# Kernel optimization log

Measured on AMD Instinct MI355X. Metric: run time of the kernel, lower is better.

Reference implementation:

```python
import jax, jax.numpy as jnp
import numpy as np

B, L, D, H = 2, 2048, 1024, 16
Dh = D // H

def setup_inputs() -> dict:
    key = jax.random.key(0)
    kx, kq, kk, kv, ko = jax.random.split(key, 5)
    scale = 1.0 / np.sqrt(D)
    return {
        "x": jax.random.normal(kx, (B, L, D), dtype=jnp.float32),
        "Wq": jax.random.normal(kq, (D, H, Dh), dtype=jnp.float32) * scale,
        "Wk": jax.random.normal(kk, (D, H, Dh), dtype=jnp.float32) * scale,
        "Wv": jax.random.normal(kv, (D, H, Dh), dtype=jnp.float32) * scale,
        "Wout": jax.random.normal(ko, (H, Dh, D), dtype=jnp.float32) * (1.0 / np.sqrt(D)),
    }

def reference(x, Wq, Wk, Wv, Wout):
    # QKV projections: [B,L,D] x [D,H,Dh] -> [B,L,H,Dh]
    q = jnp.einsum('bld,dhe->blhe', x, Wq)
    k = jnp.einsum('bld,dhe->blhe', x, Wk)
    v = jnp.einsum('bld,dhe->blhe', x, Wv)
    # scores [B,H,L,L]
    a = jnp.einsum('bqhd,bkhd->bhqk', q, k) / (Dh ** 0.5)
    Lq = x.shape[1]
    mask = jnp.tril(jnp.ones((1, 1, Lq, Lq), dtype=jnp.bool_))
    NEG_INF = jnp.finfo(jnp.float32).min
    a = jnp.where(mask, a, NEG_INF)
    a = jax.nn.softmax(a, axis=-1)
    o = jnp.einsum('bhqk,bkhd->bqhd', a, v)
    # output projection: [B,L,H,Dh] x [H,Dh,D] -> [B,L,D]
    return jnp.einsum('blhe,hed->bld', o, Wout)
```

## Files before the change

kernel.cpp:

```cpp
#include <hip/hip_runtime.h>

typedef __bf16 bf16x8 __attribute__((ext_vector_type(8)));
typedef __bf16 bf16x4 __attribute__((ext_vector_type(4)));
typedef float  floatx4 __attribute__((ext_vector_type(4)));

constexpr int Bc = 2, Lc = 2048, Dc = 1024, Hc = 16, Dhc = 64;
constexpr int Mr = 4096;

__device__ __forceinline__ void gl_lds16(const void* g, void* l) {
  __builtin_amdgcn_global_load_lds(
      (const __attribute__((address_space(1))) void*)g,
      (__attribute__((address_space(3))) void*)l, 16, 0, 0);
}

__global__ __launch_bounds__(256) void k_pack_rows(const float* __restrict__ X,
                                                   __bf16* __restrict__ P) {
  __shared__ __align__(16) __bf16 tile[64][32];
  int t = threadIdx.x;
  int m0 = blockIdx.x * 64, p0 = blockIdx.y * 4;
  int r = t >> 2, cc = t & 3;
  const float4* src = (const float4*)&X[(size_t)(m0 + r) * 1024 + p0 * 8 + cc * 8];
  float4 v0 = src[0], v1 = src[1];
  bf16x8 o;
  o[0] = (__bf16)v0.x; o[1] = (__bf16)v0.y; o[2] = (__bf16)v0.z; o[3] = (__bf16)v0.w;
  o[4] = (__bf16)v1.x; o[5] = (__bf16)v1.y; o[6] = (__bf16)v1.z; o[7] = (__bf16)v1.w;
  *(bf16x8*)&tile[r][cc * 8] = o;
  __syncthreads();
  int pc = t >> 6, ml = t & 63;
  bf16x8 q = *(bf16x8*)&tile[ml][pc * 8];
  *(bf16x8*)&P[((size_t)(p0 + pc) * Mr + m0 + ml) * 8] = q;
}

__global__ __launch_bounds__(256) void k_pack_T4(const float* __restrict__ W0,
                                                 const float* __restrict__ W1,
                                                 const float* __restrict__ W2,
                                                 const float* __restrict__ W3,
                                                 __bf16* __restrict__ Pall) {
  int z = blockIdx.z;
  const float* W = (z == 0) ? W0 : (z == 1) ? W1 : (z == 2) ? W2 : W3;
  __bf16* P = Pall + (size_t)z * 1024 * 1024;
  __shared__ __align__(16) __bf16 tile[64][66];
  int t = threadIdx.x;
  int k0 = blockIdx.x * 64, n0 = blockIdx.y * 64;
  int r = t >> 2, cc = t & 3;
  const float4* src = (const float4*)&W[(size_t)(k0 + r) * 1024 + n0 + cc * 16];
#pragma unroll
  for (int i = 0; i < 4; i++) {
    float4 v = src[i];
    tile[r][cc * 16 + i * 4 + 0] = (__bf16)v.x;
    tile[r][cc * 16 + i * 4 + 1] = (__bf16)v.y;
    tile[r][cc * 16 + i * 4 + 2] = (__bf16)v.z;
    tile[r][cc * 16 + i * 4 + 3] = (__bf16)v.w;
  }
  __syncthreads();
#pragma unroll
  for (int i = 0; i < 2; i++) {
    int c = t + i * 256;
    int pl = c >> 6, nl = c & 63;
    bf16x8 o;
#pragma unroll
    for (int j = 0; j < 8; j++) o[j] = tile[pl * 8 + j][nl];
    *(bf16x8*)&P[((size_t)(k0 / 8 + pl) * 1024 + n0 + nl) * 8] = o;
  }
}

template <int MODE, int AM>
__global__ __launch_bounds__(256) void k_gemm(const __bf16* __restrict__ Ap8,
                                              const __bf16* __restrict__ Bp8,
                                              float* __restrict__ outF,
                                              __bf16* __restrict__ Qb,
                                              __bf16* __restrict__ Kb,
                                              __bf16* __restrict__ Vb) {
  constexpr int K = 1024;
  constexpr int KCB = 2080;
  __shared__ __align__(16) char smem[4 * KCB * 4];
  char* As_raw = smem;
  char* Bs_raw = smem + 4 * KCB;
  int t = threadIdx.x, lane = t & 63, w = t >> 6;
  int quad = lane >> 4, l16 = lane & 15;
  int m0 = blockIdx.x * 128;
  const __bf16* Bbase;
  int n0loc, mat = 0;
  if (MODE == 1) {
    mat = blockIdx.y >> 3;
    Bbase = Bp8 + (size_t)mat * 1024 * 1024;
    n0loc = (blockIdx.y & 7) * 128;
  } else {
    Bbase = Bp8;
    n0loc = blockIdx.y * 128;
  }
  int wm = (w & 1) * 64, wn = (w >> 1) * 64;
  floatx4 acc[4][4] = {};

  for (int k0 = 0; k0 < K; k0 += 32) {
    int kp = k0 >> 3;
    const __bf16* ga = Ap8 + ((size_t)(kp + w) * AM + m0 + lane) * 8;
    const __bf16* gb = Bbase + ((size_t)(kp + w) * 1024 + n0loc + lane) * 8;
    char* la = As_raw + w * KCB;
    char* lb = Bs_raw + w * KCB;
    __syncthreads();
    gl_lds16(ga, la);
    gl_lds16(ga + 512, la + 1024);
    gl_lds16(gb, lb);
    gl_lds16(gb + 512, lb + 1024);
    __syncthreads();
    bf16x8 af[4], bfv[4];
#pragma unroll
    for (int mi = 0; mi < 4; mi++)
      af[mi] = *(const bf16x8*)(As_raw + quad * KCB + (wm + mi * 16 + l16) * 16);
#pragma unroll
    for (int ni = 0; ni < 4; ni++)
      bfv[ni] = *(const bf16x8*)(Bs_raw + quad * KCB + (wn + ni * 16 + l16) * 16);
#pragma unroll
    for (int mi = 0; mi < 4; mi++)
#pragma unroll
      for (int ni = 0; ni < 4; ni++)
        acc[mi][ni] = __builtin_amdgcn_mfma_f32_16x16x32_bf16(af[mi], bfv[ni], acc[mi][ni], 0, 0, 0);
  }

  __syncthreads();

  if (MODE == 0) {
    float* slf = (float*)(smem + w * (4 * KCB));
#pragma unroll
    for (int nh = 0; nh < 2; nh++) {
#pragma unroll
      for (int mi = 0; mi < 4; mi++)
#pragma unroll
        for (int nin = 0; nin < 2; nin++)
#pragma unroll
          for (int r = 0; r < 4; r++) {
            int l_loc = mi * 16 + quad * 4 + r;
            int c_loc = nin * 16 + l16;
            slf[l_loc * 32 + c_loc] = acc[mi][nh * 2 + nin][r];
          }
      __builtin_amdgcn_s_waitcnt(0);
#pragma unroll
      for (int i = 0; i < 8; i++) {
        int c = i * 64 + lane;
        float4 v = *(float4*)((char*)slf + c * 16);
        int row = c >> 3, sub = c & 7;
        *(float4*)&outF[(size_t)(m0 + wm + row) * 1024 + n0loc + wn + nh * 32 + sub * 4] = v;
      }
      if (nh == 0) __builtin_amdgcn_s_waitcnt(0);
    }
  } else {
    __bf16* sl = (__bf16*)(smem + w * (4 * KCB));
    int b = (m0 + wm) >> 11;
    int lbase = (m0 + wm) & 2047;
    int h = (n0loc + wn) >> 6;
    int bh2 = b * 16 + h;
    __bf16* dst;
    float scl = 1.0f;
    if (mat == 0) {
      dst = Qb + (((size_t)(bh2 * 64 + (lbase >> 5)) * 4) << 9);
      scl = 0.18033688011112042f;
    } else if (mat == 1) {
      dst = Kb + (((size_t)(bh2 * 32 + (lbase >> 6)) * 8) << 9);
    } else {
      dst = Vb + (((size_t)(bh2 * 32 + (lbase >> 6)) * 8) << 9);
    }
#pragma unroll
    for (int mi = 0; mi < 4; mi++)
#pragma unroll
      for (int ni = 0; ni < 4; ni++)
#pragma unroll
        for (int r = 0; r < 4; r++) {
          int l_loc = mi * 16 + quad * 4 + r;
          int e = ni * 16 + l16;
          int off;
          if (mat == 0)
            off = ((l_loc >> 5) * 4 + ((l_loc >> 4) & 1) * 2 + (e >> 5)) * 512 +
                  (((e >> 3) & 3) * 16 + (l_loc & 15)) * 8 + (e & 7);
          else if (mat == 1)
            off = ((l_loc >> 4) * 2 + (e >> 5)) * 512 +
                  (((e >> 3) & 3) * 16 + (l_loc & 15)) * 8 + (e & 7);
          else
            off = ((e >> 4) * 2 + (l_loc >> 5)) * 512 +
                  (((l_loc >> 2) & 3) * 16 + (e & 15)) * 8 + ((l_loc >> 4) & 1) * 4 + (l_loc & 3);
          sl[off] = (__bf16)(acc[mi][ni][r] * scl);
        }
    __builtin_amdgcn_s_waitcnt(0);
#pragma unroll
    for (int i = 0; i < 8; i++) {
      int c = i * 64 + lane;
      bf16x8 v = *(bf16x8*)(sl + c * 8);
      *(bf16x8*)(dst + c * 8) = v;
    }
  }
}

__global__ __launch_bounds__(256) void k_attn(const __bf16* __restrict__ Qf,
                                              const __bf16* __restrict__ Kf,
                                              const __bf16* __restrict__ Vf,
                                              __bf16* __restrict__ Op8) {
  __shared__ float PO[4][64][33];
  __shared__ float Pl[4][2][16];
  int t = threadIdx.x;
  int lane = t & 63, w = t >> 6;
  int quad = lane >> 4, l16 = lane & 15;
  int bid = blockIdx.x;
  int xcd = bid & 7, g = bid >> 3;
  int bh = xcd * 4 + (g & 3);
  int qt = 63 - (g >> 2);
  int qbase = qt * 32;

  const __bf16* Qp = Qf + (((size_t)(bh * 64 + qt) * 4) << 9) + lane * 8;
  bf16x8 qf[2][2];
#pragma unroll
  for (int mi = 0; mi < 2; mi++)
#pragma unroll
    for (int kk = 0; kk < 2; kk++)
      qf[mi][kk] = *(const bf16x8*)(Qp + ((mi * 2 + kk) << 9));

  floatx4 ot[4][2] = {};
  float l_s[2] = {0.f, 0.f};

  auto do_tile = [&](int kt, bool domask) {
    int kbase = kt * 64;
    const __bf16* Kp = Kf + (((size_t)(bh * 32 + kt) * 8) << 9) + lane * 8;
    const __bf16* Vp = Vf + (((size_t)(bh * 32 + kt) * 8) << 9) + lane * 8;
    bf16x8 ka[4][2], va[4][2];
#pragma unroll
    for (int kb = 0; kb < 4; kb++)
#pragma unroll
      for (int kk = 0; kk < 2; kk++) {
        ka[kb][kk] = *(const bf16x8*)(Kp + ((kb * 2 + kk) << 9));
        va[kb][kk] = *(const bf16x8*)(Vp + ((kb * 2 + kk) << 9));
      }

    floatx4 st[4][2] = {};
#pragma unroll
    for (int kb = 0; kb < 4; kb++)
#pragma unroll
      for (int mi = 0; mi < 2; mi++) {
        st[kb][mi] = __builtin_amdgcn_mfma_f32_16x16x32_bf16(ka[kb][0], qf[mi][0], st[kb][mi], 0, 0, 0);
        st[kb][mi] = __builtin_amdgcn_mfma_f32_16x16x32_bf16(ka[kb][1], qf[mi][1], st[kb][mi], 0, 0, 0);
      }

    bf16x8 pb[2][2];
#pragma unroll
    for (int mi = 0; mi < 2; mi++) {
      int q_g = qbase + mi * 16 + l16;
      float pv[4][4];
      float psum = 0.f;
#pragma unroll
      for (int kb = 0; kb < 4; kb++)
#pragma unroll
        for (int r = 0; r < 4; r++) {
          float v = st[kb][mi][r];
          if (domask) {
            int key = kbase + kb * 16 + quad * 4 + r;
            if (key > q_g) v = -__builtin_inff();
          }
          float p = __builtin_amdgcn_exp2f(v);
          pv[kb][r] = p;
          psum += p;
        }
      l_s[mi] += psum;
#pragma unroll
      for (int kp = 0; kp < 2; kp++) {
        bf16x8 p8;
#pragma unroll
        for (int j = 0; j < 4; j++) {
          p8[j] = (__bf16)pv[kp * 2][j];
          p8[j + 4] = (__bf16)pv[kp * 2 + 1][j];
        }
        pb[mi][kp] = p8;
      }
    }

#pragma unroll
    for (int kbd = 0; kbd < 4; kbd++)
#pragma unroll
      for (int mi = 0; mi < 2; mi++) {
        ot[kbd][mi] = __builtin_amdgcn_mfma_f32_16x16x32_bf16(va[kbd][0], pb[mi][0], ot[kbd][mi], 0, 0, 0);
        ot[kbd][mi] = __builtin_amdgcn_mfma_f32_16x16x32_bf16(va[kbd][1], pb[mi][1], ot[kbd][mi], 0, 0, 0);
      }
  };

  int nkt = ((qt * 32 + 31) >> 6) + 1;
  for (int kt = w; kt < nkt - 1; kt += 4) do_tile(kt, false);
  if (((nkt - 1) & 3) == w) do_tile(nkt - 1, true);

#pragma unroll
  for (int mi = 0; mi < 2; mi++) {
    l_s[mi] += __shfl_xor(l_s[mi], 16);
    l_s[mi] += __shfl_xor(l_s[mi], 32);
  }

#pragma unroll
  for (int mi = 0; mi < 2; mi++) {
    if (quad == 0) Pl[w][mi][l16] = l_s[mi];
#pragma unroll
    for (int kbd = 0; kbd < 4; kbd++)
#pragma unroll
      for (int r = 0; r < 4; r++)
        PO[w][kbd * 16 + quad * 4 + r][mi * 16 + l16] = ot[kbd][mi][r];
  }
  __syncthreads();

  int oct = lane >> 3, rl = lane & 7;
  int ql = w * 8 + rl;
  float lstar = 0.f;
#pragma unroll
  for (int ww = 0; ww < 4; ww++) lstar += Pl[ww][ql >> 4][ql & 15];
  float inv = 1.f / lstar;
  bf16x8 ov;
#pragma unroll
  for (int j = 0; j < 8; j++) {
    float accv = 0.f;
#pragma unroll
    for (int ww = 0; ww < 4; ww++) accv += PO[ww][oct * 8 + j][ql];
    ov[j] = (__bf16)(accv * inv);
  }
  int b = bh >> 4, h = bh & 15;
  size_t row = (size_t)b * Lc + qbase + ql;
  *(bf16x8*)&Op8[((size_t)(h * 8 + oct) * Mr + row) * 8] = ov;
}

extern "C" void kernel_launch(void* const* d_in, const int* in_sizes, int n_in,
                              void* d_out, int out_size, void* d_ws, size_t ws_size,
                              hipStream_t stream) {
  const float* x  = (const float*)d_in[0];
  const float* Wq = (const float*)d_in[1];
  const float* Wk = (const float*)d_in[2];
  const float* Wv = (const float*)d_in[3];
  const float* Wo = (const float*)d_in[4];
  float* out = (float*)d_out;

  if (ws_size < (size_t)50331648) return;
  __bf16* xb   = (__bf16*)d_ws;
  __bf16* wqkv = xb + (size_t)Mr * Dc;
  __bf16* wot  = wqkv + (size_t)3 * Dc * Dc;
  __bf16* Qfr  = wot + (size_t)Dc * Dc;
  __bf16* Kfr  = Qfr + (size_t)Mr * Dc;
  __bf16* Vfr  = Kfr + (size_t)Mr * Dc;
  __bf16* Op8  = Vfr + (size_t)Mr * Dc;

  k_pack_rows<<<dim3(64, 32), 256, 0, stream>>>(x, xb);
  k_pack_T4<<<dim3(16, 16, 4), 256, 0, stream>>>(Wq, Wk, Wv, Wo, wqkv);

  k_gemm<1, Mr><<<dim3(32, 24), 256, 0, stream>>>(xb, wqkv, nullptr, Qfr, Kfr, Vfr);

  k_attn<<<dim3(2048), 256, 0, stream>>>(Qfr, Kfr, Vfr, Op8);

  k_gemm<0, Mr><<<dim3(32, 8), 256, 0, stream>>>(Op8, wot, out, nullptr, nullptr, nullptr);
}
```

Measured before the change: 168.1 us.

## Merge pack kernels, retile output GEMM, shrink attention reduction LDS

The two packing kernels become one launch indexed by a flat block id, which removes a launch. The output-projection GEMM is split into its own kernel with 128x64 tiles, doubling the grid from 256 to 512 blocks to fill more CUs. The attention kernel's cross-wave partial-output reduction moves from a padded fp32 LDS buffer to a bf16 transposed buffer read as 8-wide vectors, and gets a launch_bounds occupancy hint of 5. The bf16 partials add rounding error before the final sum.

```diff
diff --git a/kernel.cpp b/kernel.cpp
--- a/kernel.cpp
+++ b/kernel.cpp
@@ -13,64 +13,63 @@
       (__attribute__((address_space(3))) void*)l, 16, 0, 0);
 }
 
-__global__ __launch_bounds__(256) void k_pack_rows(const float* __restrict__ X,
-                                                   __bf16* __restrict__ P) {
-  __shared__ __align__(16) __bf16 tile[64][32];
+__global__ __launch_bounds__(256) void k_pack(const float* __restrict__ X,
+                                              const float* __restrict__ W0,
+                                              const float* __restrict__ W1,
+                                              const float* __restrict__ W2,
+                                              const float* __restrict__ W3,
+                                              __bf16* __restrict__ Pw,
+                                              __bf16* __restrict__ Px) {
+  __shared__ __align__(16) __bf16 tile[64][66];
+  int bid = blockIdx.x;
   int t = threadIdx.x;
-  int m0 = blockIdx.x * 64, p0 = blockIdx.y * 4;
-  int r = t >> 2, cc = t & 3;
-  const float4* src = (const float4*)&X[(size_t)(m0 + r) * 1024 + p0 * 8 + cc * 8];
-  float4 v0 = src[0], v1 = src[1];
-  bf16x8 o;
-  o[0] = (__bf16)v0.x; o[1] = (__bf16)v0.y; o[2] = (__bf16)v0.z; o[3] = (__bf16)v0.w;
-  o[4] = (__bf16)v1.x; o[5] = (__bf16)v1.y; o[6] = (__bf16)v1.z; o[7] = (__bf16)v1.w;
-  *(bf16x8*)&tile[r][cc * 8] = o;
-  __syncthreads();
-  int pc = t >> 6, ml = t & 63;
-  bf16x8 q = *(bf16x8*)&tile[ml][pc * 8];
-  *(bf16x8*)&P[((size_t)(p0 + pc) * Mr + m0 + ml) * 8] = q;
-}
-
-__global__ __launch_bounds__(256) void k_pack_T4(const float* __restrict__ W0,
-                                                 const float* __restrict__ W1,
-                                                 const float* __restrict__ W2,
-                                                 const float* __restrict__ W3,
-                                                 __bf16* __restrict__ Pall) {
-  int z = blockIdx.z;
-  const float* W = (z == 0) ? W0 : (z == 1) ? W1 : (z == 2) ? W2 : W3;
-  __bf16* P = Pall + (size_t)z * 1024 * 1024;
-  __shared__ __align__(16) __bf16 tile[64][66];
-  int t = threadIdx.x;
-  int k0 = blockIdx.x * 64, n0 = blockIdx.y * 64;
-  int r = t >> 2, cc = t & 3;
-  const float4* src = (const float4*)&W[(size_t)(k0 + r) * 1024 + n0 + cc * 16];
-#pragma unroll
-  for (int i = 0; i < 4; i++) {
-    float4 v = src[i];
-    tile[r][cc * 16 + i * 4 + 0] = (__bf16)v.x;
-    tile[r][cc * 16 + i * 4 + 1] = (__bf16)v.y;
-    tile[r][cc * 16 + i * 4 + 2] = (__bf16)v.z;
-    tile[r][cc * 16 + i * 4 + 3] = (__bf16)v.w;
-  }
-  __syncthreads();
-#pragma unroll
-  for (int i = 0; i < 2; i++) {
-    int c = t + i * 256;
-    int pl = c >> 6, nl = c & 63;
+  if (bid < 1024) {
+    int z = bid >> 8, rem = bid & 255;
+    int k0 = (rem & 15) << 6, n0 = (rem >> 4) << 6;
+    const float* W = (z == 0) ? W0 : (z == 1) ? W1 : (z == 2) ? W2 : W3;
+    __bf16* P = Pw + (size_t)z * 1024 * 1024;
+    int r = t >> 2, cc = t & 3;
+    const float4* src = (const float4*)&W[(size_t)(k0 + r) * 1024 + n0 + cc * 16];
+#pragma unroll
+    for (int i = 0; i < 4; i++) {
+      float4 v = src[i];
+      tile[r][cc * 16 + i * 4 + 0] = (__bf16)v.x;
+      tile[r][cc * 16 + i * 4 + 1] = (__bf16)v.y;
+      tile[r][cc * 16 + i * 4 + 2] = (__bf16)v.z;
+      tile[r][cc * 16 + i * 4 + 3] = (__bf16)v.w;
+    }
+    __syncthreads();
+#pragma unroll
+    for (int i = 0; i < 2; i++) {
+      int c = t + i * 256;
+      int pl = c >> 6, nl = c & 63;
+      bf16x8 o;
+#pragma unroll
+      for (int j = 0; j < 8; j++) o[j] = tile[pl * 8 + j][nl];
+      *(bf16x8*)&P[((size_t)(k0 / 8 + pl) * 1024 + n0 + nl) * 8] = o;
+    }
+  } else {
+    int xid = bid - 1024;
+    int m0 = (xid & 63) << 6, p0 = (xid >> 6) << 2;
+    int r = t >> 2, cc = t & 3;
+    const float4* src = (const float4*)&X[(size_t)(m0 + r) * 1024 + p0 * 8 + cc * 8];
+    float4 v0 = src[0], v1 = src[1];
     bf16x8 o;
-#pragma unroll
-    for (int j = 0; j < 8; j++) o[j] = tile[pl * 8 + j][nl];
-    *(bf16x8*)&P[((size_t)(k0 / 8 + pl) * 1024 + n0 + nl) * 8] = o;
-  }
-}
-
-template <int MODE, int AM>
-__global__ __launch_bounds__(256) void k_gemm(const __bf16* __restrict__ Ap8,
-                                              const __bf16* __restrict__ Bp8,
-                                              float* __restrict__ outF,
-                                              __bf16* __restrict__ Qb,
-                                              __bf16* __restrict__ Kb,
-                                              __bf16* __restrict__ Vb) {
+    o[0] = (__bf16)v0.x; o[1] = (__bf16)v0.y; o[2] = (__bf16)v0.z; o[3] = (__bf16)v0.w;
+    o[4] = (__bf16)v1.x; o[5] = (__bf16)v1.y; o[6] = (__bf16)v1.z; o[7] = (__bf16)v1.w;
+    *(bf16x8*)&tile[0][r * 32 + cc * 8] = o;
+    __syncthreads();
+    int pc = t >> 6, ml = t & 63;
+    bf16x8 q = *(bf16x8*)&tile[0][ml * 32 + pc * 8];
+    *(bf16x8*)&Px[((size_t)(p0 + pc) * Mr + m0 + ml) * 8] = q;
+  }
+}
+
+__global__ __launch_bounds__(256) void k_gemm_qkv(const __bf16* __restrict__ Ap8,
+                                                  const __bf16* __restrict__ Bp8,
+                                                  __bf16* __restrict__ Qb,
+                                                  __bf16* __restrict__ Kb,
+                                                  __bf16* __restrict__ Vb) {
   constexpr int K = 1024;
   constexpr int KCB = 2080;
   __shared__ __align__(16) char smem[4 * KCB * 4];
@@ -79,22 +78,15 @@
   int t = threadIdx.x, lane = t & 63, w = t >> 6;
   int quad = lane >> 4, l16 = lane & 15;
   int m0 = blockIdx.x * 128;
-  const __bf16* Bbase;
-  int n0loc, mat = 0;
-  if (MODE == 1) {
-    mat = blockIdx.y >> 3;
-    Bbase = Bp8 + (size_t)mat * 1024 * 1024;
-    n0loc = (blockIdx.y & 7) * 128;
-  } else {
-    Bbase = Bp8;
-    n0loc = blockIdx.y * 128;
-  }
+  int mat = blockIdx.y >> 3;
+  const __bf16* Bbase = Bp8 + (size_t)mat * 1024 * 1024;
+  int n0loc = (blockIdx.y & 7) * 128;
   int wm = (w & 1) * 64, wn = (w >> 1) * 64;
   floatx4 acc[4][4] = {};
 
   for (int k0 = 0; k0 < K; k0 += 32) {
     int kp = k0 >> 3;
-    const __bf16* ga = Ap8 + ((size_t)(kp + w) * AM + m0 + lane) * 8;
+    const __bf16* ga = Ap8 + ((size_t)(kp + w) * Mr + m0 + lane) * 8;
     const __bf16* gb = Bbase + ((size_t)(kp + w) * 1024 + n0loc + lane) * 8;
     char* la = As_raw + w * KCB;
     char* lb = Bs_raw + w * KCB;
@@ -120,81 +112,114 @@
 
   __syncthreads();
 
-  if (MODE == 0) {
-    float* slf = (float*)(smem + w * (4 * KCB));
-#pragma unroll
-    for (int nh = 0; nh < 2; nh++) {
-#pragma unroll
-      for (int mi = 0; mi < 4; mi++)
-#pragma unroll
-        for (int nin = 0; nin < 2; nin++)
-#pragma unroll
-          for (int r = 0; r < 4; r++) {
-            int l_loc = mi * 16 + quad * 4 + r;
-            int c_loc = nin * 16 + l16;
-            slf[l_loc * 32 + c_loc] = acc[mi][nh * 2 + nin][r];
-          }
-      __builtin_amdgcn_s_waitcnt(0);
-#pragma unroll
-      for (int i = 0; i < 8; i++) {
-        int c = i * 64 + lane;
-        float4 v = *(float4*)((char*)slf + c * 16);
-        int row = c >> 3, sub = c & 7;
-        *(float4*)&outF[(size_t)(m0 + wm + row) * 1024 + n0loc + wn + nh * 32 + sub * 4] = v;
-      }
-      if (nh == 0) __builtin_amdgcn_s_waitcnt(0);
-    }
+  __bf16* sl = (__bf16*)(smem + w * (4 * KCB));
+  int b = (m0 + wm) >> 11;
+  int lbase = (m0 + wm) & 2047;
+  int h = (n0loc + wn) >> 6;
+  int bh2 = b * 16 + h;
+  __bf16* dst;
+  float scl = 1.0f;
+  if (mat == 0) {
+    dst = Qb + (((size_t)(bh2 * 64 + (lbase >> 5)) * 4) << 9);
+    scl = 0.18033688011112042f;
+  } else if (mat == 1) {
+    dst = Kb + (((size_t)(bh2 * 32 + (lbase >> 6)) * 8) << 9);
   } else {
-    __bf16* sl = (__bf16*)(smem + w * (4 * KCB));
-    int b = (m0 + wm) >> 11;
-    int lbase = (m0 + wm) & 2047;
-    int h = (n0loc + wn) >> 6;
-    int bh2 = b * 16 + h;
-    __bf16* dst;
-    float scl = 1.0f;
-    if (mat == 0) {
-      dst = Qb + (((size_t)(bh2 * 64 + (lbase >> 5)) * 4) << 9);
-      scl = 0.18033688011112042f;
-    } else if (mat == 1) {
-      dst = Kb + (((size_t)(bh2 * 32 + (lbase >> 6)) * 8) << 9);
-    } else {
-      dst = Vb + (((size_t)(bh2 * 32 + (lbase >> 6)) * 8) << 9);
-    }
-#pragma unroll
-    for (int mi = 0; mi < 4; mi++)
+    dst = Vb + (((size_t)(bh2 * 32 + (lbase >> 6)) * 8) << 9);
+  }
+#pragma unroll
+  for (int mi = 0; mi < 4; mi++)
+#pragma unroll
+    for (int ni = 0; ni < 4; ni++)
+#pragma unroll
+      for (int r = 0; r < 4; r++) {
+        int l_loc = mi * 16 + quad * 4 + r;
+        int e = ni * 16 + l16;
+        int off;
+        if (mat == 0)
+          off = ((l_loc >> 5) * 4 + ((l_loc >> 4) & 1) * 2 + (e >> 5)) * 512 +
+                (((e >> 3) & 3) * 16 + (l_loc & 15)) * 8 + (e & 7);
+        else if (mat == 1)
+          off = ((l_loc >> 4) * 2 + (e >> 5)) * 512 +
+                (((e >> 3) & 3) * 16 + (l_loc & 15)) * 8 + (e & 7);
+        else
+          off = ((e >> 4) * 2 + (l_loc >> 5)) * 512 +
+                (((l_loc >> 2) & 3) * 16 + (e & 15)) * 8 + ((l_loc >> 4) & 1) * 4 + (l_loc & 3);
+        sl[off] = (__bf16)(acc[mi][ni][r] * scl);
+      }
+  __builtin_amdgcn_s_waitcnt(0);
+#pragma unroll
+  for (int i = 0; i < 8; i++) {
+    int c = i * 64 + lane;
+    bf16x8 v = *(bf16x8*)(sl + c * 8);
+    *(bf16x8*)(dst + c * 8) = v;
+  }
+}
+
+__global__ __launch_bounds__(256) void k_gemm_out(const __bf16* __restrict__ Ap8,
+                                                  const __bf16* __restrict__ Bp8,
+                                                  float* __restrict__ outF) {
+  constexpr int K = 1024;
+  constexpr int KCB_A = 2080;
+  constexpr int KCB_B = 1056;
+  __shared__ __align__(16) char smem[33792];
+  char* As_raw = smem;
+  char* Bs_raw = smem + 4 * KCB_A;
+  int t = threadIdx.x, lane = t & 63, w = t >> 6;
+  int quad = lane >> 4, l16 = lane & 15;
+  int m0 = blockIdx.x * 128, n0 = blockIdx.y * 64;
+  int wm = w * 32;
+  floatx4 acc[2][4] = {};
+
+  for (int k0 = 0; k0 < K; k0 += 32) {
+    int kp = k0 >> 3;
+    const __bf16* ga = Ap8 + ((size_t)(kp + w) * Mr + m0 + lane) * 8;
+    const __bf16* gb = Bp8 + ((size_t)(kp + w) * 1024 + n0 + lane) * 8;
+    char* la = As_raw + w * KCB_A;
+    char* lb = Bs_raw + w * KCB_B;
+    __syncthreads();
+    gl_lds16(ga, la);
+    gl_lds16(ga + 512, la + 1024);
+    gl_lds16(gb, lb);
+    __syncthreads();
+    bf16x8 af[2], bfv[4];
+#pragma unroll
+    for (int mi = 0; mi < 2; mi++)
+      af[mi] = *(const bf16x8*)(As_raw + quad * KCB_A + (wm + mi * 16 + l16) * 16);
+#pragma unroll
+    for (int ni = 0; ni < 4; ni++)
+      bfv[ni] = *(const bf16x8*)(Bs_raw + quad * KCB_B + (ni * 16 + l16) * 16);
+#pragma unroll
+    for (int mi = 0; mi < 2; mi++)
 #pragma unroll
       for (int ni = 0; ni < 4; ni++)
-#pragma unroll
-        for (int r = 0; r < 4; r++) {
-          int l_loc = mi * 16 + quad * 4 + r;
-          int e = ni * 16 + l16;
-          int off;
-          if (mat == 0)
-            off = ((l_loc >> 5) * 4 + ((l_loc >> 4) & 1) * 2 + (e >> 5)) * 512 +
-                  (((e >> 3) & 3) * 16 + (l_loc & 15)) * 8 + (e & 7);
-          else if (mat == 1)
-            off = ((l_loc >> 4) * 2 + (e >> 5)) * 512 +
-                  (((e >> 3) & 3) * 16 + (l_loc & 15)) * 8 + (e & 7);
-          else
-            off = ((e >> 4) * 2 + (l_loc >> 5)) * 512 +
-                  (((l_loc >> 2) & 3) * 16 + (e & 15)) * 8 + ((l_loc >> 4) & 1) * 4 + (l_loc & 3);
-          sl[off] = (__bf16)(acc[mi][ni][r] * scl);
-        }
-    __builtin_amdgcn_s_waitcnt(0);
-#pragma unroll
-    for (int i = 0; i < 8; i++) {
-      int c = i * 64 + lane;
-      bf16x8 v = *(bf16x8*)(sl + c * 8);
-      *(bf16x8*)(dst + c * 8) = v;
-    }
-  }
-}
-
-__global__ __launch_bounds__(256) void k_attn(const __bf16* __restrict__ Qf,
-                                              const __bf16* __restrict__ Kf,
-                                              const __bf16* __restrict__ Vf,
-                                              __bf16* __restrict__ Op8) {
-  __shared__ float PO[4][64][33];
+        acc[mi][ni] = __builtin_amdgcn_mfma_f32_16x16x32_bf16(af[mi], bfv[ni], acc[mi][ni], 0, 0, 0);
+  }
+
+  __syncthreads();
+  float* slf = (float*)(smem + w * 8448);
+#pragma unroll
+  for (int mi = 0; mi < 2; mi++)
+#pragma unroll
+    for (int ni = 0; ni < 4; ni++)
+#pragma unroll
+      for (int r = 0; r < 4; r++)
+        slf[(mi * 16 + quad * 4 + r) * 66 + ni * 16 + l16] = acc[mi][ni][r];
+  __builtin_amdgcn_s_waitcnt(0);
+#pragma unroll
+  for (int i = 0; i < 8; i++) {
+    int c = i * 64 + lane;
+    int row = c >> 4, sub = c & 15;
+    float4 v = *(float4*)(slf + row * 66 + sub * 4);
+    *(float4*)&outF[(size_t)(m0 + wm + row) * 1024 + n0 + sub * 4] = v;
+  }
+}
+
+__global__ __launch_bounds__(256, 5) void k_attn(const __bf16* __restrict__ Qf,
+                                                 const __bf16* __restrict__ Kf,
+                                                 const __bf16* __restrict__ Vf,
+                                                 __bf16* __restrict__ Op8) {
+  __shared__ __align__(16) __bf16 POt[4][32][72];
   __shared__ float Pl[4][2][16];
   int t = threadIdx.x;
   int lane = t & 63, w = t >> 6;
@@ -293,10 +318,12 @@
   for (int mi = 0; mi < 2; mi++) {
     if (quad == 0) Pl[w][mi][l16] = l_s[mi];
 #pragma unroll
-    for (int kbd = 0; kbd < 4; kbd++)
-#pragma unroll
-      for (int r = 0; r < 4; r++)
-        PO[w][kbd * 16 + quad * 4 + r][mi * 16 + l16] = ot[kbd][mi][r];
+    for (int kbd = 0; kbd < 4; kbd++) {
+      bf16x4 p4;
+#pragma unroll
+      for (int r = 0; r < 4; r++) p4[r] = (__bf16)ot[kbd][mi][r];
+      *(bf16x4*)&POt[w][mi * 16 + l16][kbd * 16 + quad * 4] = p4;
+    }
   }
   __syncthreads();
 
@@ -306,14 +333,16 @@
 #pragma unroll
   for (int ww = 0; ww < 4; ww++) lstar += Pl[ww][ql >> 4][ql & 15];
   float inv = 1.f / lstar;
+  float accv[8] = {};
+#pragma unroll
+  for (int ww = 0; ww < 4; ww++) {
+    bf16x8 pv8 = *(const bf16x8*)&POt[ww][ql][oct * 8];
+#pragma unroll
+    for (int j = 0; j < 8; j++) accv[j] += (float)pv8[j];
+  }
   bf16x8 ov;
 #pragma unroll
-  for (int j = 0; j < 8; j++) {
-    float accv = 0.f;
-#pragma unroll
-    for (int ww = 0; ww < 4; ww++) accv += PO[ww][oct * 8 + j][ql];
-    ov[j] = (__bf16)(accv * inv);
-  }
+  for (int j = 0; j < 8; j++) ov[j] = (__bf16)(accv[j] * inv);
   int b = bh >> 4, h = bh & 15;
   size_t row = (size_t)b * Lc + qbase + ql;
   *(bf16x8*)&Op8[((size_t)(h * 8 + oct) * Mr + row) * 8] = ov;
@@ -338,12 +367,11 @@
   __bf16* Vfr  = Kfr + (size_t)Mr * Dc;
   __bf16* Op8  = Vfr + (size_t)Mr * Dc;
 
-  k_pack_rows<<<dim3(64, 32), 256, 0, stream>>>(x, xb);
-  k_pack_T4<<<dim3(16, 16, 4), 256, 0, stream>>>(Wq, Wk, Wv, Wo, wqkv);
-
-  k_gemm<1, Mr><<<dim3(32, 24), 256, 0, stream>>>(xb, wqkv, nullptr, Qfr, Kfr, Vfr);
+  k_pack<<<3072, 256, 0, stream>>>(x, Wq, Wk, Wv, Wo, wqkv, xb);
+
+  k_gemm_qkv<<<dim3(32, 24), 256, 0, stream>>>(xb, wqkv, Qfr, Kfr, Vfr);
 
   k_attn<<<dim3(2048), 256, 0, stream>>>(Qfr, Kfr, Vfr, Op8);
 
-  k_gemm<0, Mr><<<dim3(32, 8), 256, 0, stream>>>(Op8, wot, out, nullptr, nullptr, nullptr);
-}
+  k_gemm_out<<<dim3(32, 16), 256, 0, stream>>>(Op8, wot, out);
+}
```

Measured after the change: 187.9 us. 11.8% more time.
